# Performance work log

Hardware: AMD Instinct MI355X
Metric: run time of the kernel (lower is better)

Reference implementation:

```python
import jax, jax.numpy as jnp
import numpy as np

B, DIM, HEADS, H, W = 4, 192, 6, 256, 256
C = DIM // HEADS  # channels per head
DN = ('NCHW', 'OIHW', 'NCHW')


def conv2d(x, w, b, padding='VALID', groups=1):
    y = jax.lax.conv_general_dilated(x, w, (1, 1), padding,
                                     dimension_numbers=DN,
                                     feature_group_count=groups)
    return y + b[None, :, None, None]


def setup_inputs() -> dict:
    key = jax.random.key(0)
    ks = jax.random.split(key, 8)
    s = 0.02
    return {
        'x': jax.random.normal(ks[0], (B, DIM, H, W), jnp.float32),
        'qkv_w': jax.random.normal(ks[1], (3 * DIM, DIM, 1, 1), jnp.float32) * s,
        'qkv_b': jnp.zeros((3 * DIM,), jnp.float32),
        'dw_w': jax.random.normal(ks[2], (3 * DIM, 1, 3, 3), jnp.float32) * s,
        'dw_b': jnp.zeros((3 * DIM,), jnp.float32),
        'proj_w': jax.random.normal(ks[3], (DIM, DIM, 1, 1), jnp.float32) * s,
        'proj_b': jnp.zeros((DIM,), jnp.float32),
        'temperature': jnp.ones((HEADS, 1, 1, 1), jnp.float32),
    }


def reference(x, qkv_w, qkv_b, dw_w, dw_b, proj_w, proj_b, temperature):
    # qkv projection: 1x1 conv then 3x3 depthwise conv
    qkv = conv2d(x, qkv_w, qkv_b)
    qkv = conv2d(qkv, dw_w, dw_b, padding='SAME', groups=3 * DIM)
    q, k, v = jnp.split(qkv, 3, axis=1)  # each (B, DIM, H, W)

    def heads(t):
        return t.reshape(B, HEADS, C, H, W)
    q, k, v = heads(q), heads(k), heads(v)

    # L2-normalize along W (matches F.normalize eps=1e-12)
    eps = 1e-12
    q = q / jnp.maximum(jnp.linalg.norm(q, axis=-1, keepdims=True), eps)
    k = k / jnp.maximum(jnp.linalg.norm(k, axis=-1, keepdims=True), eps)

    # per-channel HxH attention, contraction over W; temperature broadcasts over head
    attn = jnp.einsum('bncxw,bncyw->bncxy', q, k) * temperature  # (B,HEADS,C,H,H)
    attn = jax.nn.softmax(attn, axis=-1)
    out = jnp.einsum('bncxy,bncyw->bncxw', attn, v)  # (B,HEADS,C,H,W)

    out = out.reshape(B, DIM, H, W)
    return conv2d(out, proj_w, proj_b)
```

## Files before the change

### kernel.cpp

```cpp
#include <hip/hip_runtime.h>
#include <hip/hip_bf16.h>
#include <math.h>


#define HW 65536
#define IMW 256

typedef short bf16x8 __attribute__((ext_vector_type(8)));
typedef float f32x4  __attribute__((ext_vector_type(4)));

__device__ __forceinline__ float bf2f(ushort u) {
    return __uint_as_float((uint)u << 16);
}
__device__ __forceinline__ ushort f2bf(float f) {
    uint i = __float_as_uint(f);
    return (ushort)((i + 0x7FFFu + ((i >> 16) & 1u)) >> 16);
}

__global__ __launch_bounds__(256) void cvt_f32_bf16(const float* __restrict__ s,
                                                    ushort* __restrict__ d, int n)
{
    int i = blockIdx.x * 256 + threadIdx.x;
    if (i < n) d[i] = f2bf(s[i]);
}

__global__ __launch_bounds__(256) void cvt_transpose_f32(const float* __restrict__ src,
                                                         ushort* __restrict__ dst,
                                                         int R, int C,
                                                         long ssS, long ssD)
{
    __shared__ ushort Ls[64][72];
    int t = threadIdx.x;
    long z = blockIdx.z;
    src += z * ssS; dst += z * ssD;
    int c0 = blockIdx.x * 64, r0 = blockIdx.y * 64;
    {
        int r = t >> 2, cs = t & 3;
        const float* gp = src + (size_t)(r0 + r) * C + c0 + cs * 16;
        ushort tmp[16];
        #pragma unroll
        for (int q = 0; q < 4; ++q) {
            float4 v = *(const float4*)(gp + q * 4);
            tmp[q*4+0] = f2bf(v.x); tmp[q*4+1] = f2bf(v.y);
            tmp[q*4+2] = f2bf(v.z); tmp[q*4+3] = f2bf(v.w);
        }
        *(uint4*)&Ls[r][cs * 16]     = *(uint4*)&tmp[0];
        *(uint4*)&Ls[r][cs * 16 + 8] = *(uint4*)&tmp[8];
    }
    __syncthreads();
    {
        int cc = t & 63, seg = t >> 6;
        ushort tmp[16];
        #pragma unroll
        for (int j = 0; j < 16; ++j) tmp[j] = Ls[seg * 16 + j][cc];
        ushort* op = dst + (size_t)(c0 + cc) * R + r0 + seg * 16;
        *(uint4*)(op)     = *(uint4*)&tmp[0];
        *(uint4*)(op + 8) = *(uint4*)&tmp[8];
    }
}

__global__ __launch_bounds__(256) void transpose_bf16(const ushort* __restrict__ src,
                                                      ushort* __restrict__ dst,
                                                      int R, int C,
                                                      long ssS, long ssD)
{
    __shared__ ushort Ls[64][72];
    int t = threadIdx.x;
    long z = blockIdx.z;
    src += z * ssS; dst += z * ssD;
    int c0 = blockIdx.x * 64, r0 = blockIdx.y * 64;
    {
        int r = t >> 2, cs = t & 3;
        const ushort* gp = src + (size_t)(r0 + r) * C + c0 + cs * 16;
        *(uint4*)&Ls[r][cs * 16]     = *(const uint4*)(gp);
        *(uint4*)&Ls[r][cs * 16 + 8] = *(const uint4*)(gp + 8);
    }
    __syncthreads();
    {
        int cc = t & 63, seg = t >> 6;
        ushort tmp[16];
        #pragma unroll
        for (int j = 0; j < 16; ++j) tmp[j] = Ls[seg * 16 + j][cc];
        ushort* op = dst + (size_t)(c0 + cc) * R + r0 + seg * 16;
        *(uint4*)(op)     = *(uint4*)&tmp[0];
        *(uint4*)(op + 8) = *(uint4*)&tmp[8];
    }
}

__global__ __launch_bounds__(256) void transpose_v(const ushort* __restrict__ post,
                                                   ushort* __restrict__ vt)
{
    __shared__ ushort Ls[64][72];
    int t = threadIdx.x;
    int s = blockIdx.z;
    int b = s / 192, r = s - b * 192;
    const ushort* src = post + ((size_t)b * 576 + 384 + r) * HW;
    ushort*       dst = vt + (size_t)s * HW;
    int c0 = blockIdx.x * 64, r0 = blockIdx.y * 64;
    {
        int rr = t >> 2, cs = t & 3;
        const ushort* gp = src + (size_t)(r0 + rr) * IMW + c0 + cs * 16;
        *(uint4*)&Ls[rr][cs * 16]     = *(const uint4*)(gp);
        *(uint4*)&Ls[rr][cs * 16 + 8] = *(const uint4*)(gp + 8);
    }
    __syncthreads();
    {
        int cc = t & 63, seg = t >> 6;
        ushort tmp[16];
        #pragma unroll
        for (int j = 0; j < 16; ++j) tmp[j] = Ls[seg * 16 + j][cc];
        ushort* op = dst + (size_t)(c0 + cc) * IMW + r0 + seg * 16;
        *(uint4*)(op)     = *(uint4*)&tmp[0];
        *(uint4*)(op + 8) = *(uint4*)&tmp[8];
    }
}

__global__ __launch_bounds__(256) void gemm_mfma(const ushort* __restrict__ A, int lda, long sliceA,
                                                 const ushort* __restrict__ B, int ldb, long sliceB,
                                                 void* __restrict__ Dp, int ldd, long sliceD,
                                                 const float* __restrict__ bias,
                                                 int outF32, int NM, int NN)
{
    int lin = blockIdx.x;
    int r8 = lin & 7, kk_ = lin >> 3;
    int m = kk_ % NM, fg = kk_ / NM;
    int g = fg * 8 + r8;
    int nt_ = g % NN;
    long z = g / NN;
    int m0 = m * 64;

    int t = threadIdx.x, wv = t >> 6, lane = t & 63;
    int nw0 = nt_ * 256 + wv * 64;
    int fr = lane & 15, fs = (lane >> 4) * 8;
    A += z * sliceA; B += z * sliceB;

    const ushort* ap = A + (size_t)(m0 + fr) * lda + fs;
    const ushort* bp = B + (size_t)(nw0 + fr) * ldb + fs;

    f32x4 acc[4][4];
    #pragma unroll
    for (int i = 0; i < 4; ++i)
        #pragma unroll
        for (int j = 0; j < 4; ++j) acc[i][j] = (f32x4){0.f, 0.f, 0.f, 0.f};

    #pragma unroll 2
    for (int k0 = 0; k0 < 192; k0 += 32) {
        bf16x8 a[4], b[4];
        #pragma unroll
        for (int i = 0; i < 4; ++i)
            a[i] = *(const bf16x8*)(ap + (size_t)(i * 16) * lda + k0);
        #pragma unroll
        for (int j = 0; j < 4; ++j)
            b[j] = *(const bf16x8*)(bp + (size_t)(j * 16) * ldb + k0);
        #pragma unroll
        for (int i = 0; i < 4; ++i)
            #pragma unroll
            for (int j = 0; j < 4; ++j)
                acc[i][j] = __builtin_amdgcn_mfma_f32_16x16x32_bf16(a[i], b[j], acc[i][j], 0, 0, 0);
    }

    int rbase = (lane >> 4) * 4;
    if (outF32) {
        float* D = (float*)Dp + z * sliceD;
        #pragma unroll
        for (int i = 0; i < 4; ++i) {
            #pragma unroll
            for (int r_ = 0; r_ < 4; ++r_) {
                int mrow = m0 + i * 16 + rbase + r_;
                float bv = bias ? bias[mrow] : 0.f;
                #pragma unroll
                for (int j = 0; j < 4; ++j)
                    D[(size_t)mrow * ldd + nw0 + j * 16 + fr] = acc[i][j][r_] + bv;
            }
        }
    } else {
        ushort* D = (ushort*)Dp + z * sliceD;
        #pragma unroll
        for (int i = 0; i < 4; ++i) {
            #pragma unroll
            for (int r_ = 0; r_ < 4; ++r_) {
                int mrow = m0 + i * 16 + rbase + r_;
                float bv = bias ? bias[mrow] : 0.f;
                #pragma unroll
                for (int j = 0; j < 4; ++j)
                    D[(size_t)mrow * ldd + nw0 + j * 16 + fr] = f2bf(acc[i][j][r_] + bv);
            }
        }
    }
}

__global__ __launch_bounds__(256) void attn_fused(const ushort* __restrict__ post,
                                                  const ushort* __restrict__ vt,
                                                  const float* __restrict__ temp,
                                                  ushort* __restrict__ O)
{
    __shared__ ushort Ws[64][40];
    __shared__ ushort Xs[256][40];
    __shared__ ushort Ps[64][264];
    int t = threadIdx.x, wv = t >> 6, lane = t & 63;
    int lin = blockIdx.x;
    int r8 = lin & 7, k_ = lin >> 3;
    int mtile = k_ & 3, fg = k_ >> 2;
    int s = fg * 8 + r8;
    int b = s / 192, ch = s - b * 192;
    const ushort* Aq = post + ((size_t)b * 576 + ch) * HW;
    const ushort* Bk = Aq + (size_t)192 * HW;
    const ushort* Vt = vt + (size_t)s * HW;
    int m0 = mtile * 64;

    f32x4 acc[16];
    #pragma unroll
    for (int i = 0; i < 16; ++i) acc[i] = (f32x4){0.f, 0.f, 0.f, 0.f};

    for (int k0 = 0; k0 < 256; k0 += 32) {
        {   int r = t >> 2, ss = t & 3;
            *(uint4*)&Ws[r][ss * 8] =
                *(const uint4*)(Aq + (size_t)(m0 + r) * IMW + k0 + ss * 8);
        }
        {   const ushort* bp = Bk + (size_t)t * IMW + k0;
            #pragma unroll
            for (int ss = 0; ss < 4; ++ss)
                *(uint4*)&Xs[t][ss * 8] = *(const uint4*)(bp + ss * 8);
        }
        __syncthreads();
        bf16x8 a = *(const bf16x8*)&Ws[wv * 16 + (lane & 15)][(lane >> 4) * 8];
        #pragma unroll
        for (int nt = 0; nt < 16; ++nt) {
            bf16x8 bfrag = *(const bf16x8*)&Xs[nt * 16 + (lane & 15)][(lane >> 4) * 8];
            acc[nt] = __builtin_amdgcn_mfma_f32_16x16x32_bf16(a, bfrag, acc[nt], 0, 0, 0);
        }
        __syncthreads();
    }

    float tv = temp[ch >> 5];
    #pragma unroll
    for (int r_ = 0; r_ < 4; ++r_) {
        float v[16];
        float mx = -3.4e38f;
        #pragma unroll
        for (int nt = 0; nt < 16; ++nt) { v[nt] = acc[nt][r_] * tv; mx = fmaxf(mx, v[nt]); }
        #pragma unroll
        for (int sh = 1; sh < 16; sh <<= 1) mx = fmaxf(mx, __shfl_xor(mx, sh, 64));
        float sum = 0.f;
        #pragma unroll
        for (int nt = 0; nt < 16; ++nt) { v[nt] = __expf(v[nt] - mx); sum += v[nt]; }
        #pragma unroll
        for (int sh = 1; sh < 16; sh <<= 1) sum += __shfl_xor(sum, sh, 64);
        float inv = 1.f / sum;
        int ml = wv * 16 + (lane >> 4) * 4 + r_;
        #pragma unroll
        for (int nt = 0; nt < 16; ++nt)
            Ps[ml][(lane & 15) + nt * 16] = f2bf(v[nt] * inv);
    }

    f32x4 acc2[16];
    #pragma unroll
    for (int i = 0; i < 16; ++i) acc2[i] = (f32x4){0.f, 0.f, 0.f, 0.f};

    for (int y0 = 0; y0 < 256; y0 += 32) {
        {   const ushort* bp = Vt + (size_t)t * IMW + y0;
            #pragma unroll
            for (int ss = 0; ss < 4; ++ss)
                *(uint4*)&Xs[t][ss * 8] = *(const uint4*)(bp + ss * 8);
        }
        __syncthreads();
        bf16x8 a = *(const bf16x8*)&Ps[wv * 16 + (lane & 15)][y0 + (lane >> 4) * 8];
        #pragma unroll
        for (int nt = 0; nt < 16; ++nt) {
            bf16x8 bfrag = *(const bf16x8*)&Xs[nt * 16 + (lane & 15)][(lane >> 4) * 8];
            acc2[nt] = __builtin_amdgcn_mfma_f32_16x16x32_bf16(a, bfrag, acc2[nt], 0, 0, 0);
        }
        __syncthreads();
    }

    ushort* Op = O + (size_t)s * HW;
    int mrow = m0 + wv * 16 + (lane >> 4) * 4;
    int ncol = lane & 15;
    #pragma unroll
    for (int r_ = 0; r_ < 4; ++r_) {
        #pragma unroll
        for (int nt = 0; nt < 16; ++nt)
            Op[(size_t)(mrow + r_) * IMW + ncol + nt * 16] = f2bf(acc2[nt][r_]);
    }
}

__global__ __launch_bounds__(256) void dw3x3_l2norm(const ushort* __restrict__ in,
                                                    const float* __restrict__ w,
                                                    const float* __restrict__ bias,
                                                    ushort* __restrict__ out)
{
    int t = threadIdx.x;
    int lane = t & 63, wv = t >> 6;
    int ch = blockIdx.y;
    int r0 = blockIdx.x * 16 + wv * 4;
    const ushort* img  = in  + ((size_t)blockIdx.z * 576 + ch) * HW;
    ushort*       outp = out + ((size_t)blockIdx.z * 576 + ch) * HW;
    int px = lane * 4;

    float rv[6][4], lv[6], rx[6];
    #pragma unroll
    for (int i = 0; i < 6; ++i) {
        int rr = r0 - 1 + i;
        if ((unsigned)rr <= 255u) {
            ushort4 cv = *(const ushort4*)&img[(size_t)rr * IMW + px];
            rv[i][0] = bf2f(cv.x); rv[i][1] = bf2f(cv.y);
            rv[i][2] = bf2f(cv.z); rv[i][3] = bf2f(cv.w);
        } else {
            rv[i][0] = rv[i][1] = rv[i][2] = rv[i][3] = 0.f;
        }
        float l = __shfl_up(rv[i][3], 1, 64);
        lv[i] = (lane == 0) ? 0.f : l;
        float r = __shfl_down(rv[i][0], 1, 64);
        rx[i] = (lane == 63) ? 0.f : r;
    }

    const float* wch = w + ch * 9;
    float bv = bias[ch];
    bool do_norm = (ch < 384);

    #pragma unroll
    for (int j = 0; j < 4; ++j) {
        float a0 = bv, a1 = bv, a2 = bv, a3 = bv;
        #pragma unroll
        for (int dy = 0; dy < 3; ++dy) {
            int i = j + dy;
            float w0 = wch[dy * 3], w1 = wch[dy * 3 + 1], w2 = wch[dy * 3 + 2];
            a0 += lv[i]    * w0 + rv[i][0] * w1 + rv[i][1] * w2;
            a1 += rv[i][0] * w0 + rv[i][1] * w1 + rv[i][2] * w2;
            a2 += rv[i][1] * w0 + rv[i][2] * w1 + rv[i][3] * w2;
            a3 += rv[i][2] * w0 + rv[i][3] * w1 + rx[i]    * w2;
        }
        if (do_norm) {
            float ss = a0 * a0 + a1 * a1 + a2 * a2 + a3 * a3;
            #pragma unroll
            for (int m = 1; m < 64; m <<= 1) ss += __shfl_xor(ss, m, 64);
            float inv = 1.0f / fmaxf(sqrtf(ss), 1e-12f);
            a0 *= inv; a1 *= inv; a2 *= inv; a3 *= inv;
        }
        ushort4 o;
        o.x = f2bf(a0); o.y = f2bf(a1); o.z = f2bf(a2); o.w = f2bf(a3);
        *(ushort4*)&outp[(size_t)(r0 + j) * IMW + px] = o;
    }
}

extern "C" void kernel_launch(void* const* d_in, const int* in_sizes, int n_in,
                              void* d_out, int out_size, void* d_ws, size_t ws_size,
                              hipStream_t stream)
{
    const float* x      = (const float*)d_in[0];
    const float* qkv_w  = (const float*)d_in[1];
    const float* qkv_b  = (const float*)d_in[2];
    const float* dw_w   = (const float*)d_in[3];
    const float* dw_b   = (const float*)d_in[4];
    const float* proj_w = (const float*)d_in[5];
    const float* proj_b = (const float*)d_in[6];
    const float* temp   = (const float*)d_in[7];
    float* out = (float*)d_out;

    const size_t off_wq   = 0;
    const size_t off_wp   = 110592;
    const size_t off_pre  = 262144;
    const size_t off_post = off_pre + (size_t)4 * 576 * HW;
    const size_t off_xt   = off_post + (size_t)4 * 576 * HW;
    const size_t total_us = off_xt + (size_t)4 * 192 * HW;
    if (ws_size < total_us * sizeof(ushort)) return;

    ushort* wsb  = (ushort*)d_ws;
    ushort* wq   = wsb + off_wq;
    ushort* wp   = wsb + off_wp;
    ushort* pre  = wsb + off_pre;
    ushort* post = wsb + off_post;
    ushort* xt   = wsb + off_xt;
    ushort* Obuf = pre;
    ushort* Otb  = pre + (size_t)4 * 192 * HW;

    const long SL = (long)192 * HW;

    cvt_f32_bf16<<<dim3(432), 256, 0, stream>>>(qkv_w, wq, 110592);
    cvt_f32_bf16<<<dim3(144), 256, 0, stream>>>(proj_w, wp, 36864);

    cvt_transpose_f32<<<dim3(1024, 3, 4), 256, 0, stream>>>(x, xt, 192, HW, SL, SL);
    gemm_mfma<<<dim3(9 * 256 * 4), 256, 0, stream>>>(wq, 192, 0, xt, 192, SL,
                                                     pre, HW, (long)576 * HW,
                                                     qkv_b, 0, 9, 256);
    dw3x3_l2norm<<<dim3(16, 576, 4), 256, 0, stream>>>(pre, dw_w, dw_b, post);
    transpose_v<<<dim3(4, 4, 768), 256, 0, stream>>>(post, xt);
    attn_fused<<<dim3(4 * 768), 256, 0, stream>>>(post, xt, temp, Obuf);
    transpose_bf16<<<dim3(1024, 3, 4), 256, 0, stream>>>(Obuf, Otb, 192, HW, SL, SL);
    gemm_mfma<<<dim3(3 * 256 * 4), 256, 0, stream>>>(wp, 192, 0, Otb, 192, SL,
                                                     out, HW, SL,
                                                     proj_b, 1, 3, 256);
}
```

Measured before the change: 822.6 us.

## Stage GEMM B tile through LDS with register double-buffered prefetch

In the MFMA GEMM, each thread now loads one contiguous 64-byte row chunk of the B operand into registers and writes it into a shared-memory tile, replacing the earlier strided per-lane global reads. The next k-slice of both A and B is prefetched into registers while the current slice is consumed, which overlaps global loads with MFMA work. The aim is better-coalesced global access and hidden load latency, paid for with two barriers per k-step and extra LDS traffic. The padded row stride of 40 elements is meant to reduce bank conflicts.

```diff
diff --git a/kernel.cpp b/kernel.cpp
--- a/kernel.cpp
+++ b/kernel.cpp
@@ -129,13 +129,13 @@
     long z = g / NN;
     int m0 = m * 64;
 
+    __shared__ ushort Xs[256][40];
     int t = threadIdx.x, wv = t >> 6, lane = t & 63;
-    int nw0 = nt_ * 256 + wv * 64;
     int fr = lane & 15, fs = (lane >> 4) * 8;
     A += z * sliceA; B += z * sliceB;
 
-    const ushort* ap = A + (size_t)(m0 + fr) * lda + fs;
-    const ushort* bp = B + (size_t)(nw0 + fr) * ldb + fs;
+    const ushort* bstage = B + (size_t)(nt_ * 256 + t) * ldb;
+    const ushort* ap     = A + (size_t)(m0 + fr) * lda + fs;
 
     f32x4 acc[4][4];
     #pragma unroll
@@ -143,22 +143,39 @@
         #pragma unroll
         for (int j = 0; j < 4; ++j) acc[i][j] = (f32x4){0.f, 0.f, 0.f, 0.f};
 
-    #pragma unroll 2
-    for (int k0 = 0; k0 < 192; k0 += 32) {
-        bf16x8 a[4], b[4];
-        #pragma unroll
-        for (int i = 0; i < 4; ++i)
-            a[i] = *(const bf16x8*)(ap + (size_t)(i * 16) * lda + k0);
-        #pragma unroll
-        for (int j = 0; j < 4; ++j)
-            b[j] = *(const bf16x8*)(bp + (size_t)(j * 16) * ldb + k0);
-        #pragma unroll
-        for (int i = 0; i < 4; ++i)
-            #pragma unroll
-            for (int j = 0; j < 4; ++j)
-                acc[i][j] = __builtin_amdgcn_mfma_f32_16x16x32_bf16(a[i], b[j], acc[i][j], 0, 0, 0);
-    }
-
+    uint4 bs[4];
+    bf16x8 a_cur[4], a_nxt[4];
+    #pragma unroll
+    for (int c = 0; c < 4; ++c) bs[c] = *(const uint4*)(bstage + c * 8);
+    #pragma unroll
+    for (int i = 0; i < 4; ++i) a_cur[i] = *(const bf16x8*)(ap + (size_t)(i * 16) * lda);
+
+    for (int kit = 0; kit < 6; ++kit) {
+        int k0 = kit * 32;
+        #pragma unroll
+        for (int c = 0; c < 4; ++c) *(uint4*)&Xs[t][c * 8] = bs[c];
+        if (kit < 5) {
+            #pragma unroll
+            for (int c = 0; c < 4; ++c)
+                bs[c] = *(const uint4*)(bstage + k0 + 32 + c * 8);
+            #pragma unroll
+            for (int i = 0; i < 4; ++i)
+                a_nxt[i] = *(const bf16x8*)(ap + (size_t)(i * 16) * lda + k0 + 32);
+        }
+        __syncthreads();
+        #pragma unroll
+        for (int j = 0; j < 4; ++j) {
+            bf16x8 b = *(const bf16x8*)&Xs[wv * 64 + j * 16 + fr][fs];
+            #pragma unroll
+            for (int i = 0; i < 4; ++i)
+                acc[i][j] = __builtin_amdgcn_mfma_f32_16x16x32_bf16(a_cur[i], b, acc[i][j], 0, 0, 0);
+        }
+        __syncthreads();
+        #pragma unroll
+        for (int i = 0; i < 4; ++i) a_cur[i] = a_nxt[i];
+    }
+
+    int nw0 = nt_ * 256 + wv * 64;
     int rbase = (lane >> 4) * 4;
     if (outF32) {
         float* D = (float*)Dp + z * sliceD;
```

Measured after the change: 989.7 us. 1.2x slower.
